# Kernel optimization log

Hardware: AMD Instinct MI355X
Metric: run time of the kernel (lower is better)

## Reference

```python
import jax, jax.numpy as jnp
import numpy as np

B, D, E, H, A = 4096, 1024, 8, 1024, 512  # batch, state_dim, num_options, num_neurons, num_actions


def setup_inputs() -> dict:
    key = jax.random.key(0)
    ks = jax.random.split(key, 16)
    s = 0.02
    return {
        "state": jax.random.normal(ks[0], (B, D), jnp.float32),
        "selected_options": jax.random.randint(ks[1], (B,), 0, E, jnp.int32),
        # option network: Linear(D,H) -> ReLU -> Linear(H,E)
        "Wo1": jax.random.normal(ks[2], (D, H), jnp.float32) * s,
        "bo1": jnp.zeros((H,), jnp.float32),
        "Wo2": jax.random.normal(ks[3], (H, E), jnp.float32) * s,
        "bo2": jnp.zeros((E,), jnp.float32),
        # E expert nets, each: Linear(D,H)+ReLU -> Linear(H,H)+ReLU -> Linear(H,A)
        "We1": jax.random.normal(ks[4], (E, D, H), jnp.float32) * s,
        "be1": jnp.zeros((E, H), jnp.float32),
        "We2": jax.random.normal(ks[5], (E, H, H), jnp.float32) * s,
        "be2": jnp.zeros((E, H), jnp.float32),
        "We3": jax.random.normal(ks[6], (E, H, A), jnp.float32) * s,
        "be3": jnp.zeros((E, A), jnp.float32),
        # termination network: Linear(D,H) -> ReLU -> Linear(H,1) -> Sigmoid
        "Wt1": jax.random.normal(ks[7], (D, H), jnp.float32) * s,
        "bt1": jnp.zeros((H,), jnp.float32),
        "Wt2": jax.random.normal(ks[8], (H, 1), jnp.float32) * s,
        "bt2": jnp.zeros((1,), jnp.float32),
    }


def reference(state, selected_options, Wo1, bo1, Wo2, bo2,
              We1, be1, We2, be2, We3, be3, Wt1, bt1, Wt2, bt2):
    # option head
    option_probs = jax.nn.softmax(jnp.maximum(state @ Wo1 + bo1, 0.0) @ Wo2 + bo2, axis=-1)

    # expert MLPs: compute all experts vectorized, then gather per-sample selected expert.
    # (the torch code loops per sample; equal action sizes so no padding is needed)
    h = jnp.maximum(jnp.einsum("bd,edh->beh", state, We1) + be1, 0.0)   # [B,E,H]
    h = jnp.maximum(jnp.einsum("beh,ehk->bek", h, We2) + be2, 0.0)      # [B,E,H]
    logits = jnp.einsum("beh,eha->bea", h, We3) + be3                   # [B,E,A]
    probs_all = jax.nn.softmax(logits, axis=-1)
    sel = selected_options[:, None, None]
    action_probs = jnp.take_along_axis(probs_all, sel, axis=1)[:, 0, :]  # [B,A]
    selected_actions = jnp.argmax(action_probs, axis=-1)

    # termination head
    termination_prob = jax.nn.sigmoid(jnp.maximum(state @ Wt1 + bt1, 0.0) @ Wt2 + bt2)

    return option_probs, action_probs, termination_prob, selected_options, selected_actions
```

## Files before the change

### kernel.cpp

```cpp
#include <hip/hip_runtime.h>
#include <hip/hip_bf16.h>

#define B_ 4096
#define D_ 1024
#define E_ 8
#define H_ 1024
#define A_ 512
#define PB 6144
#define NTT 24
#define FB_CAP 128
#define FROWS (E_ * FB_CAP)
#define KSPLIT 4
#define MARGIN 3.0e-3f

typedef __attribute__((ext_vector_type(8))) short s16x8;
typedef __attribute__((ext_vector_type(4))) float f32x4;

__device__ __forceinline__ unsigned short f2bf(float f) {
    __hip_bfloat16 h = __float2bfloat16(f);
    return *reinterpret_cast<unsigned short*>(&h);
}
__device__ __forceinline__ float bf2f(unsigned short u) {
    return __uint_as_float(((unsigned int)u) << 16);
}
__device__ __forceinline__ void gload16(const void* g, void* l) {
    __builtin_amdgcn_global_load_lds(
        (const __attribute__((address_space(1))) unsigned int*)g,
        (__attribute__((address_space(3))) unsigned int*)l, 16, 0, 0);
}

__global__ void k_prep(const float* __restrict__ x, unsigned short* __restrict__ y,
                       const float* __restrict__ Wo1, const float* __restrict__ Wt1,
                       unsigned short* __restrict__ Wbf,
                       const int* __restrict__ sel, int* __restrict__ tile_expert,
                       int* __restrict__ rowlist, int* __restrict__ pos_of_row,
                       int* __restrict__ rowlist2, int* __restrict__ cur2) {
    const int t = threadIdx.x;
    if (blockIdx.x > 4096) {
        int j = (blockIdx.x - 4097) * 256 + t;
        float4 v;
        if (j < 262144) v = ((const float4*)Wo1)[j];
        else            v = ((const float4*)Wt1)[j - 262144];
        ushort4 o;
        o.x = f2bf(v.x); o.y = f2bf(v.y); o.z = f2bf(v.z); o.w = f2bf(v.w);
        ((ushort4*)Wbf)[j] = o;
        return;
    }
    if (blockIdx.x > 0) {
        int i = (blockIdx.x - 1) * 256 + t;
        float4 v = ((const float4*)x)[i];
        ushort4 o;
        o.x = f2bf(v.x); o.y = f2bf(v.y); o.z = f2bf(v.z); o.w = f2bf(v.w);
        ((ushort4*)y)[i] = o;
        return;
    }
    __shared__ int scnt[E_], soff[E_], scur[E_];
    if (t < E_) { scnt[t] = 0; scur[t] = 0; cur2[t] = 0; }
    for (int i = t; i < PB; i += 256) rowlist[i] = -1;
    for (int i = t; i < FROWS; i += 256) rowlist2[i] = -1;
    __syncthreads();
    for (int b = t; b < B_; b += 256) {
        int e = sel[b]; e = e < 0 ? 0 : (e >= E_ ? E_ - 1 : e);
        atomicAdd(&scnt[e], 1);
    }
    __syncthreads();
    if (t == 0) {
        int off = 0;
        for (int e = 0; e < E_; ++e) {
            soff[e] = off;
            int tiles = (scnt[e] + 255) >> 8;
            for (int k = 0; k < tiles; ++k) tile_expert[(off >> 8) + k] = e;
            off += tiles << 8;
        }
        for (int k = off >> 8; k < NTT; ++k) tile_expert[k] = -1;
    }
    __syncthreads();
    for (int b = t; b < B_; b += 256) {
        int e = sel[b]; e = e < 0 ? 0 : (e >= E_ ? E_ - 1 : e);
        int pos = atomicAdd(&scur[e], 1);
        int p = soff[e] + pos; if (p >= PB) p = PB - 1;
        rowlist[p] = b;
        pos_of_row[b] = p;
    }
}

template<int TN, int WBF>
__device__ __forceinline__ void gemm2(
    const unsigned short* __restrict__ g0, const unsigned short* __restrict__ g1,
    const unsigned short* __restrict__ g2, const unsigned short* __restrict__ g3,
    const void* __restrict__ Wp, int Nw, const float* __restrict__ bp,
    unsigned short* __restrict__ Cbf, float* __restrict__ Cf, int Ncols, int relu,
    unsigned short* As, unsigned short* Bs)
{
    constexpr int NI = TN / 32;
    constexpr int BL = TN / 8;
    constexpr int BT = TN * 64;
    const int t = threadIdx.x, lane = t & 63, w = t >> 6;
    const int wr = w >> 1, wc = w & 1;
    const int n_loc = t & (TN - 1);
    const int kg = (t / TN) * BL;
    const float* wcolf = (const float*)Wp + n_loc;
    const unsigned short* wcolu = (const unsigned short*)Wp + n_loc;
    const int aseg = w * 2048 + lane * 8;

    f32x4 acc[4][NI];
#pragma unroll
    for (int i = 0; i < 4; ++i)
#pragma unroll
        for (int j = 0; j < NI; ++j)
#pragma unroll
            for (int r = 0; r < 4; ++r) acc[i][j][r] = 0.f;

    float bregf[BL];
    unsigned short bregu[BL];

#define G_STAGE_A(IT, BUF) {                                                 \
        const int o_ = (BUF) * 16384 + aseg;                                 \
        const int ko_ = (IT) * 64;                                           \
        gload16(g0 + ko_, As + o_);                                          \
        gload16(g1 + ko_, As + o_ + 512);                                    \
        gload16(g2 + ko_, As + o_ + 1024);                                   \
        gload16(g3 + ko_, As + o_ + 1536);                                   \
    }

#define G_LOAD_B(IT) {                                                       \
        if constexpr (WBF) {                                                 \
            _Pragma("unroll")                                                \
            for (int i_ = 0; i_ < BL; ++i_)                                  \
                bregu[i_] = wcolu[(size_t)((IT) * 64 + kg + i_) * Nw];       \
        } else {                                                             \
            _Pragma("unroll")                                                \
            for (int i_ = 0; i_ < BL; ++i_)                                  \
                bregf[i_] = wcolf[(size_t)((IT) * 64 + kg + i_) * Nw];       \
        }                                                                    \
    }

#define G_PACK_B(BUF) {                                                      \
        unsigned int u_[BL / 2];                                             \
        if constexpr (WBF) {                                                 \
            _Pragma("unroll")                                                \
            for (int j_ = 0; j_ < BL / 2; ++j_)                              \
                u_[j_] = (unsigned)bregu[2 * j_] | ((unsigned)bregu[2 * j_ + 1] << 16); \
        } else {                                                             \
            _Pragma("unroll")                                                \
            for (int j_ = 0; j_ < BL / 2; ++j_)                              \
                u_[j_] = ((unsigned)f2bf(bregf[2 * j_ + 1]) << 16) | (unsigned)f2bf(bregf[2 * j_]); \
        }                                                                    \
        _Pragma("unroll")                                                    \
        for (int j_ = 0; j_ < BL / 8; ++j_) {                                \
            const int cj_ = (kg >> 3) + j_;                                  \
            uint4 v_;                                                        \
            v_.x = u_[4 * j_]; v_.y = u_[4 * j_ + 1];                        \
            v_.z = u_[4 * j_ + 2]; v_.w = u_[4 * j_ + 3];                    \
            *(uint4*)&Bs[(BUF) * BT + n_loc * 64 + ((cj_ ^ (n_loc & 7)) << 3)] = v_; \
        }                                                                    \
    }

    G_STAGE_A(0, 0);
    G_LOAD_B(0);
    G_PACK_B(0);
    __syncthreads();

    for (int it = 0; it < 16; ++it) {
        const int cb = it & 1;
        if (it + 1 < 16) { G_STAGE_A(it + 1, cb ^ 1); G_LOAD_B(it + 1); }
        __builtin_amdgcn_s_setprio(1);
#pragma unroll
        for (int kq = 0; kq < 2; ++kq) {
            const int sc = kq * 4 + (lane >> 4);
            s16x8 af[4], bfr[NI];
#pragma unroll
            for (int mi = 0; mi < 4; ++mi) {
                const int ar = wr * 64 + mi * 16 + (lane & 15);
                af[mi] = *reinterpret_cast<const s16x8*>(
                    &As[cb * 16384 + ar * 64 + ((sc ^ (ar & 7)) << 3)]);
            }
#pragma unroll
            for (int ni = 0; ni < NI; ++ni) {
                const int br = wc * (TN / 2) + ni * 16 + (lane & 15);
                bfr[ni] = *reinterpret_cast<const s16x8*>(
                    &Bs[cb * BT + br * 64 + ((sc ^ (br & 7)) << 3)]);
            }
#pragma unroll
            for (int mi = 0; mi < 4; ++mi)
#pragma unroll
                for (int ni = 0; ni < NI; ++ni)
                    acc[mi][ni] = __builtin_amdgcn_mfma_f32_16x16x32_bf16(
                        af[mi], bfr[ni], acc[mi][ni], 0, 0, 0);
        }
        __builtin_amdgcn_s_setprio(0);
        if (it + 1 < 16) {
            G_PACK_B(cb ^ 1);
            __syncthreads();
        }
    }
#undef G_PACK_B
#undef G_LOAD_B
#undef G_STAGE_A

    const int cq = lane >> 4, cr = lane & 15;
#pragma unroll
    for (int ni = 0; ni < NI; ++ni) {
        const int col_l = wc * (TN / 2) + ni * 16 + cr;
        const float bv = bp[col_l];
#pragma unroll
        for (int mi = 0; mi < 4; ++mi) {
#pragma unroll
            for (int r = 0; r < 4; ++r) {
                const int row_l = wr * 64 + mi * 16 + cq * 4 + r;
                float v = acc[mi][ni][r] + bv;
                if (relu) v = fmaxf(v, 0.f);
                const size_t idx = (size_t)row_l * Ncols + col_l;
                if (Cbf) Cbf[idx] = f2bf(v);
                if (Cf)  Cf[idx] = v;
            }
        }
    }
}

__device__ __forceinline__ int a_src_chunk(int lane) { return (((lane & 7) ^ (lane >> 3)) * 8); }

__global__ __launch_bounds__(512, 2)
void k_d2(const unsigned short* __restrict__ Sbf,
          const int* __restrict__ rowlist, const int* __restrict__ tile_expert,
          const unsigned short* __restrict__ Wbf,
          const float* __restrict__ bo1, const float* __restrict__ bt1,
          const float* __restrict__ We1, const float* __restrict__ be1,
          unsigned short* __restrict__ hopt, unsigned short* __restrict__ hterm,
          unsigned short* __restrict__ h1) {
    __shared__ __align__(16) unsigned short As[2 * 16384];
    __shared__ __align__(16) unsigned short Bs[2 * 16384];
    const int t = threadIdx.x, lane = t & 63, w = t >> 6;
    const int coff = a_src_chunk(lane);
    const int r0l = w * 32 + (lane >> 3);
    const int bid = blockIdx.x;
    if (bid < 128) {
        const int nt = bid & 7, mt = bid >> 3;
        const unsigned short* g0 = Sbf + (size_t)(mt * 256 + r0l) * D_ + coff;
        const unsigned short* g1 = g0 + (size_t)8 * D_;
        const unsigned short* g2 = g0 + (size_t)16 * D_;
        const unsigned short* g3 = g0 + (size_t)24 * D_;
        const unsigned short* Wp;
        const float* bp;
        unsigned short* C;
        if (nt < 4) { Wp = Wbf + nt * 256; bp = bo1 + nt * 256;
                      C = hopt + (size_t)(mt * 256) * H_ + nt * 256; }
        else { const int n2 = (nt - 4) * 256;
               Wp = Wbf + 1048576 + n2; bp = bt1 + n2;
               C = hterm + (size_t)(mt * 256) * H_ + n2; }
        gemm2<256, 1>(g0, g1, g2, g3, Wp, H_, bp, C, nullptr, H_, 1, As, Bs);
    } else {
        const int q = bid - 128, nt = q & 3, mt = q >> 2;
        const int e = tile_expert[mt]; if (e < 0) return;
        const int base = mt * 256;
        const int sub = rowlist[base]; if (sub < 0) return;
        int r0 = rowlist[base + r0l];      if (r0 < 0) r0 = sub;
        int r1 = rowlist[base + r0l + 8];  if (r1 < 0) r1 = sub;
        int r2 = rowlist[base + r0l + 16]; if (r2 < 0) r2 = sub;
        int r3 = rowlist[base + r0l + 24]; if (r3 < 0) r3 = sub;
        const unsigned short* g0 = Sbf + (size_t)r0 * D_ + coff;
        const unsigned short* g1 = Sbf + (size_t)r1 * D_ + coff;
        const unsigned short* g2 = Sbf + (size_t)r2 * D_ + coff;
        const unsigned short* g3 = Sbf + (size_t)r3 * D_ + coff;
        gemm2<256, 0>(g0, g1, g2, g3,
                      We1 + (size_t)e * D_ * H_ + nt * 256, H_,
                      be1 + (size_t)e * H_ + nt * 256,
                      h1 + (size_t)(mt * 256) * H_ + nt * 256, nullptr, H_, 1, As, Bs);
    }
}

__global__ __launch_bounds__(512, 2)
void k_d3(const unsigned short* __restrict__ h1, const int* __restrict__ tile_expert,
          const float* __restrict__ We2, const float* __restrict__ be2,
          unsigned short* __restrict__ h2) {
    __shared__ __align__(16) unsigned short As[2 * 16384];
    __shared__ __align__(16) unsigned short Bs[2 * 8192];
    const int t = threadIdx.x, lane = t & 63, w = t >> 6;
    const int coff = a_src_chunk(lane);
    const int r0l = w * 32 + (lane >> 3);
    const int nt = blockIdx.x & 7, mt = blockIdx.x >> 3;
    const int e = tile_expert[mt]; if (e < 0) return;
    const unsigned short* g0 = h1 + (size_t)(mt * 256 + r0l) * H_ + coff;
    gemm2<128, 0>(g0, g0 + (size_t)8 * H_, g0 + (size_t)16 * H_, g0 + (size_t)24 * H_,
                  We2 + (size_t)e * H_ * H_ + nt * 128, H_,
                  be2 + (size_t)e * H_ + nt * 128,
                  h2 + (size_t)(mt * 256) * H_ + nt * 128, nullptr, H_, 1, As, Bs);
}

__global__ __launch_bounds__(512, 2)
void k_d5(const unsigned short* __restrict__ h2, const int* __restrict__ tile_expert,
          const float* __restrict__ We3, const float* __restrict__ be3,
          float* __restrict__ lgt) {
    __shared__ __align__(16) unsigned short As[2 * 16384];
    __shared__ __align__(16) unsigned short Bs[2 * 4096];
    const int t = threadIdx.x, lane = t & 63, w = t >> 6;
    const int coff = a_src_chunk(lane);
    const int r0l = w * 32 + (lane >> 3);
    const int nt = blockIdx.x & 7, mt = blockIdx.x >> 3;
    const int e = tile_expert[mt]; if (e < 0) return;
    const unsigned short* g0 = h2 + (size_t)(mt * 256 + r0l) * H_ + coff;
    gemm2<64, 0>(g0, g0 + (size_t)8 * H_, g0 + (size_t)16 * H_, g0 + (size_t)24 * H_,
                 We3 + (size_t)e * H_ * A_ + nt * 64, A_,
                 be3 + (size_t)e * A_ + nt * 64,
                 nullptr, lgt + (size_t)(mt * 256) * A_ + nt * 64, A_, 0, As, Bs);
}

__device__ __forceinline__ void opt_body(int b, const unsigned short* __restrict__ h,
                                         const float* __restrict__ Wo2, const float* __restrict__ bo2,
                                         float* __restrict__ out, float* sm) {
    const int t = threadIdx.x;
    float acc[E_];
#pragma unroll
    for (int j = 0; j < E_; ++j) acc[j] = 0.f;
    for (int k = t; k < H_; k += 256) {
        float hv = bf2f(h[(size_t)b * H_ + k]);
#pragma unroll
        for (int j = 0; j < E_; ++j) acc[j] = fmaf(hv, Wo2[k * E_ + j], acc[j]);
    }
#pragma unroll
    for (int j = 0; j < E_; ++j)
        for (int off = 32; off; off >>= 1) acc[j] += __shfl_down(acc[j], off, 64);
    float* red = sm;
    float* probs = sm + 4 * E_;
    int wave = t >> 6, lane = t & 63;
    if (lane == 0)
        for (int j = 0; j < E_; ++j) red[wave * E_ + j] = acc[j];
    __syncthreads();
    if (t == 0) {
        float z[E_]; float m = -1e30f;
        for (int j = 0; j < E_; ++j) {
            z[j] = red[j] + red[E_ + j] + red[2 * E_ + j] + red[3 * E_ + j] + bo2[j];
            m = fmaxf(m, z[j]);
        }
        float s = 0.f;
        for (int j = 0; j < E_; ++j) { z[j] = expf(z[j] - m); s += z[j]; }
        float inv = 1.f / s;
        for (int j = 0; j < E_; ++j) probs[j] = z[j] * inv;
    }
    __syncthreads();
    if (t < E_) out[(size_t)b * E_ + t] = probs[t];
}

__device__ __forceinline__ void term_body(int b, const unsigned short* __restrict__ h,
                                          const float* __restrict__ Wt2, const float* __restrict__ bt2,
                                          float* __restrict__ out, float* sm) {
    const int t = threadIdx.x;
    float acc = 0.f;
    for (int k = t; k < H_; k += 256) acc = fmaf(bf2f(h[(size_t)b * H_ + k]), Wt2[k], acc);
    for (int off = 32; off; off >>= 1) acc += __shfl_down(acc, off, 64);
    if ((t & 63) == 0) sm[t >> 6] = acc;
    __syncthreads();
    if (t == 0) {
        float z = sm[0] + sm[1] + sm[2] + sm[3] + bt2[0];
        out[b] = 1.f / (1.f + expf(-z));
    }
}

__global__ __launch_bounds__(256)
void k_gather(const float* __restrict__ logits, const int* __restrict__ pos_of_row,
              const int* __restrict__ sel,
              float* __restrict__ out_probs, float* __restrict__ out_selopt,
              float* __restrict__ out_selact,
              int* __restrict__ rowlist2, int* __restrict__ cur2,
              const unsigned short* __restrict__ hopt, const float* __restrict__ Wo2,
              const float* __restrict__ bo2, float* __restrict__ out_opt,
              const unsigned short* __restrict__ hterm, const float* __restrict__ Wt2,
              const float* __restrict__ bt2, float* __restrict__ out_term) {
    __shared__ float smbuf[5 * E_ + 8];
    const int bid = blockIdx.x;
    if (bid >= 2 * B_) { term_body(bid - 2 * B_, hterm, Wt2, bt2, out_term, smbuf); return; }
    if (bid >= B_)     { opt_body(bid - B_, hopt, Wo2, bo2, out_opt, smbuf); return; }

    const int b = bid;
    int p = pos_of_row[b];
    if (p < 0) p = 0; if (p >= PB) p = PB - 1;
    const int t = threadIdx.x;
    const float* L = logits + (size_t)p * A_;
    float v0 = L[t], v1 = L[t + 256];

    float bv; int bi;
    if (v0 >= v1) { bv = v0; bi = t; } else { bv = v1; bi = t + 256; }
    for (int off = 32; off; off >>= 1) {
        float ov = __shfl_down(bv, off, 64);
        int   oi = __shfl_down(bi, off, 64);
        if (ov > bv || (ov == bv && oi < bi)) { bv = ov; bi = oi; }
    }
    __shared__ float rv[4]; __shared__ int ri[4];
    int wave = t >> 6, lane = t & 63;
    if (lane == 0) { rv[wave] = bv; ri[wave] = bi; }
    __syncthreads();
    __shared__ float sM; __shared__ int sBi;
    if (t == 0) {
        float mv = rv[0]; int mi = ri[0];
        for (int w = 1; w < 4; ++w)
            if (rv[w] > mv || (rv[w] == mv && ri[w] < mi)) { mv = rv[w]; mi = ri[w]; }
        sM = mv; sBi = mi;
    }
    __syncthreads();
    const float M = sM; const int BI = sBi;

    float e0 = expf(v0 - M), e1 = expf(v1 - M);
    float s = e0 + e1;
    for (int off = 32; off; off >>= 1) s += __shfl_down(s, off, 64);
    __shared__ float reds[4];
    if (lane == 0) reds[wave] = s;
    __syncthreads();
    float inv = 1.f / (reds[0] + reds[1] + reds[2] + reds[3]);

    out_probs[(size_t)b * A_ + t]       = e0 * inv;
    out_probs[(size_t)b * A_ + t + 256] = e1 * inv;

    float s0 = (t == BI) ? -1e30f : v0;
    float s1 = (t + 256 == BI) ? -1e30f : v1;
    float sm = fmaxf(s0, s1);
    for (int off = 32; off; off >>= 1) sm = fmaxf(sm, __shfl_down(sm, off, 64));
    __shared__ float red2[4];
    if (lane == 0) red2[wave] = sm;
    __syncthreads();

    if (t == 0) {
        float second = fmaxf(fmaxf(red2[0], red2[1]), fmaxf(red2[2], red2[3]));
        out_selact[b] = (float)BI;
        int e = sel[b]; e = e < 0 ? 0 : (e >= E_ ? E_ - 1 : e);
        out_selopt[b] = (float)sel[b];
        if (M - second < MARGIN) {
            int pos = atomicAdd(&cur2[e], 1);
            if (pos < FB_CAP) rowlist2[e * FB_CAP + pos] = b;
        }
    }
}

#define BM 64
#define BN 64
#define BK 32

__global__ __launch_bounds__(256)
void k_pgemm(const float* __restrict__ A, int lda, const int* __restrict__ flags,
             int gather, const float* __restrict__ W,
             float* __restrict__ P, int K, int N) {
    __shared__ float As_[BK][BM + 4];
    __shared__ float Bs_[BK][BN];

    const int mt = blockIdx.y, nt = blockIdx.x, kz = blockIdx.z;
    if (flags[mt * BM] < 0) return;
    const int e = mt >> 1;
    const float* Wb = W + (size_t)e * K * N + (size_t)nt * BN;

    const int t  = threadIdx.x;
    const int tx = t & 15;
    const int ty = t >> 4;

    const int arow = t >> 3;
    const int ak   = (t & 7) * 4;
    int r0 = mt * BM + arow, r1 = r0 + 32;
    if (gather) { r0 = flags[r0]; r1 = flags[r1]; }
    const int bkr = t >> 4;
    const int bn  = (t & 15) * 4;

    float acc[4][4];
#pragma unroll
    for (int i = 0; i < 4; ++i)
#pragma unroll
        for (int j = 0; j < 4; ++j) acc[i][j] = 0.0f;

    const int kbeg = kz * (K / KSPLIT);
    const int kend = kbeg + (K / KSPLIT);
    for (int k0 = kbeg; k0 < kend; k0 += BK) {
        float4 a0 = make_float4(0.f, 0.f, 0.f, 0.f), a1 = a0;
        if (r0 >= 0) a0 = *(const float4*)&A[(size_t)r0 * lda + k0 + ak];
        if (r1 >= 0) a1 = *(const float4*)&A[(size_t)r1 * lda + k0 + ak];
        float4 b0 = *(const float4*)&Wb[(size_t)(k0 + bkr) * N + bn];
        float4 b1 = *(const float4*)&Wb[(size_t)(k0 + bkr + 16) * N + bn];

        __syncthreads();
        As_[ak + 0][arow] = a0.x; As_[ak + 1][arow] = a0.y;
        As_[ak + 2][arow] = a0.z; As_[ak + 3][arow] = a0.w;
        As_[ak + 0][arow + 32] = a1.x; As_[ak + 1][arow + 32] = a1.y;
        As_[ak + 2][arow + 32] = a1.z; As_[ak + 3][arow + 32] = a1.w;
        *(float4*)&Bs_[bkr][bn]      = b0;
        *(float4*)&Bs_[bkr + 16][bn] = b1;
        __syncthreads();

#pragma unroll
        for (int kk = 0; kk < BK; ++kk) {
            const float4 av = *(const float4*)&As_[kk][ty * 4];
            const float4 bv = *(const float4*)&Bs_[kk][tx * 4];
            const float a_[4] = {av.x, av.y, av.z, av.w};
            const float b_[4] = {bv.x, bv.y, bv.z, bv.w};
#pragma unroll
            for (int i = 0; i < 4; ++i)
#pragma unroll
                for (int j = 0; j < 4; ++j)
                    acc[i][j] = fmaf(a_[i], b_[j], acc[i][j]);
        }
    }

    float* Pz = P + (size_t)kz * FROWS * N;
    const int n0 = nt * BN + tx * 4;
#pragma unroll
    for (int i = 0; i < 4; ++i) {
        int m = mt * BM + ty * 4 + i;
        *(float4*)&Pz[(size_t)m * N + n0] = make_float4(acc[i][0], acc[i][1], acc[i][2], acc[i][3]);
    }
}

__global__ __launch_bounds__(256)
void k_fred(const float* __restrict__ P, const int* __restrict__ flags,
            const float* __restrict__ bias, float* __restrict__ C, int N, int relu) {
    const int m = blockIdx.x;
    if (flags[m] < 0) return;
    const int e = m >> 7;
    const int t = threadIdx.x;
    if (t * 4 >= N) return;
    const size_t MN = (size_t)FROWS * N;
    const size_t base = (size_t)m * N + t * 4;
    float4 s = *(const float4*)&P[base];
#pragma unroll
    for (int z = 1; z < KSPLIT; ++z) {
        float4 p = *(const float4*)&P[(size_t)z * MN + base];
        s.x += p.x; s.y += p.y; s.z += p.z; s.w += p.w;
    }
    const float* bp = bias + (size_t)e * N + t * 4;
    s.x += bp[0]; s.y += bp[1]; s.z += bp[2]; s.w += bp[3];
    if (relu) {
        s.x = fmaxf(s.x, 0.f); s.y = fmaxf(s.y, 0.f);
        s.z = fmaxf(s.z, 0.f); s.w = fmaxf(s.w, 0.f);
    }
    *(float4*)&C[base] = s;
}

__global__ __launch_bounds__(256)
void k_fixup(const float* __restrict__ logitsf, const int* __restrict__ rowlist2,
             float* __restrict__ out_probs, float* __restrict__ out_selact) {
    const int i = blockIdx.x;
    const int row = rowlist2[i];
    if (row < 0) return;
    const int t = threadIdx.x;
    const float* L = logitsf + (size_t)i * A_;
    float v0 = L[t], v1 = L[t + 256];

    float bv; int bi;
    if (v0 >= v1) { bv = v0; bi = t; } else { bv = v1; bi = t + 256; }
    for (int off = 32; off; off >>= 1) {
        float ov = __shfl_down(bv, off, 64);
        int   oi = __shfl_down(bi, off, 64);
        if (ov > bv || (ov == bv && oi < bi)) { bv = ov; bi = oi; }
    }
    __shared__ float rv[4]; __shared__ int ri[4];
    int wave = t >> 6, lane = t & 63;
    if (lane == 0) { rv[wave] = bv; ri[wave] = bi; }
    __syncthreads();
    __shared__ float sM; __shared__ int sBi;
    if (t == 0) {
        float mv = rv[0]; int mi = ri[0];
        for (int w = 1; w < 4; ++w)
            if (rv[w] > mv || (rv[w] == mv && ri[w] < mi)) { mv = rv[w]; mi = ri[w]; }
        sM = mv; sBi = mi;
    }
    __syncthreads();

    float e0 = expf(v0 - sM), e1 = expf(v1 - sM);
    float s = e0 + e1;
    for (int off = 32; off; off >>= 1) s += __shfl_down(s, off, 64);
    __shared__ float reds[4];
    if (lane == 0) reds[wave] = s;
    __syncthreads();
    float inv = 1.f / (reds[0] + reds[1] + reds[2] + reds[3]);

    out_probs[(size_t)row * A_ + t]       = e0 * inv;
    out_probs[(size_t)row * A_ + t + 256] = e1 * inv;
    if (t == 0) out_selact[row] = (float)sBi;
}

extern "C" void kernel_launch(void* const* d_in, const int* in_sizes, int n_in,
                              void* d_out, int out_size, void* d_ws, size_t ws_size,
                              hipStream_t stream) {
    const float* state = (const float*)d_in[0];
    const int*   sel   = (const int*)d_in[1];
    const float* Wo1 = (const float*)d_in[2];
    const float* bo1 = (const float*)d_in[3];
    const float* Wo2 = (const float*)d_in[4];
    const float* bo2 = (const float*)d_in[5];
    const float* We1 = (const float*)d_in[6];
    const float* be1 = (const float*)d_in[7];
    const float* We2 = (const float*)d_in[8];
    const float* be2 = (const float*)d_in[9];
    const float* We3 = (const float*)d_in[10];
    const float* be3 = (const float*)d_in[11];
    const float* Wt1 = (const float*)d_in[12];
    const float* bt1 = (const float*)d_in[13];
    const float* Wt2 = (const float*)d_in[14];
    const float* bt2 = (const float*)d_in[15];
    float* out = (float*)d_out;

    char* w = (char*)d_ws;
    int* meta        = (int*)w;
    int* rowlist     = meta;
    int* pos_of_row  = meta + 6144;
    int* rowlist2    = meta + 10240;
    int* tile_expert = meta + 11264;
    int* cur2        = meta + 11296;
    char* P0 = w + 65536;
    char* P1 = P0 + 12582912;
    char* P2 = P1 + 16777216;
    unsigned short* Sbf   = (unsigned short*)P0;
    unsigned short* Wbf   = (unsigned short*)(P0 + (8u << 20));
    unsigned short* h2b   = (unsigned short*)P0;
    unsigned short* hopt  = (unsigned short*)P1;
    unsigned short* hterm = hopt + (size_t)B_ * H_;
    unsigned short* h1b   = (unsigned short*)P2;
    float* lgt  = (float*)P2;
    float* Pbuf = (float*)P1;
    float* h1f  = (float*)P0;
    float* h2f  = h1f + (size_t)FROWS * H_;
    float* lgf  = h2f + (size_t)FROWS * H_;

    size_t act_off    = (size_t)B_ * E_;
    size_t term_off   = act_off + (size_t)B_ * A_;
    size_t selopt_off = term_off + B_;
    size_t selact_off = selopt_off + B_;

    k_prep<<<6145, 256, 0, stream>>>(state, Sbf, Wo1, Wt1, Wbf, sel, tile_expert,
                                     rowlist, pos_of_row, rowlist2, cur2);

    k_d2<<<224, 512, 0, stream>>>(Sbf, rowlist, tile_expert, Wbf,
                                  bo1, bt1, We1, be1, hopt, hterm, h1b);
    k_d3<<<192, 512, 0, stream>>>(h1b, tile_expert, We2, be2, h2b);
    k_d5<<<192, 512, 0, stream>>>(h2b, tile_expert, We3, be3, lgt);

    k_gather<<<3 * B_, 256, 0, stream>>>(lgt, pos_of_row, sel,
                                         out + act_off, out + selopt_off, out + selact_off,
                                         rowlist2, cur2,
                                         hopt, Wo2, bo2, out,
                                         hterm, Wt2, bt2, out + term_off);

    k_pgemm<<<dim3(H_ / BN, FROWS / BM, KSPLIT), 256, 0, stream>>>(state, D_, rowlist2, 1, We1, Pbuf, D_, H_);
    k_fred<<<FROWS, 256, 0, stream>>>(Pbuf, rowlist2, be1, h1f, H_, 1);
    k_pgemm<<<dim3(H_ / BN, FROWS / BM, KSPLIT), 256, 0, stream>>>(h1f, H_, rowlist2, 0, We2, Pbuf, H_, H_);
    k_fred<<<FROWS, 256, 0, stream>>>(Pbuf, rowlist2, be2, h2f, H_, 1);
    k_pgemm<<<dim3(A_ / BN, FROWS / BM, KSPLIT), 256, 0, stream>>>(h2f, H_, rowlist2, 0, We3, Pbuf, H_, A_);
    k_fred<<<FROWS, 256, 0, stream>>>(Pbuf, rowlist2, be3, lgf, A_, 0);
    k_fixup<<<FROWS, 256, 0, stream>>>(lgf, rowlist2, out + act_off, out + selact_off);
}
```

Baseline: 229.6 us.

## Pre-transpose expert weights to bf16 K-major and stage B via direct LDS loads

```diff
diff --git a/kernel.cpp b/kernel.cpp
--- a/kernel.cpp
+++ b/kernel.cpp
@@ -29,25 +29,88 @@
         (__attribute__((address_space(3))) unsigned int*)l, 16, 0, 0);
 }
 
+__device__ __forceinline__ int a_src_chunk(int lane) { return (((lane & 7) ^ (lane >> 3)) * 8); }
+
+__device__ __forceinline__ int trc(int r, int c) { return (c + r + (r >> 2)) & 63; }
+
+__device__ __forceinline__ void tr_tile_256(const float* __restrict__ src, int Nsrc,
+                                            unsigned short* __restrict__ dst, float* T) {
+    const int t = threadIdx.x;
+    const int c4 = (t & 15) * 4, r0 = t >> 4;
+#pragma unroll
+    for (int i = 0; i < 8; ++i) {
+        const int r = r0 + i * 16;
+        const float4 v = *(const float4*)&src[(size_t)r * Nsrc + c4];
+        float* Tr = T + r * 64;
+        Tr[trc(r, c4 + 0)] = v.x; Tr[trc(r, c4 + 1)] = v.y;
+        Tr[trc(r, c4 + 2)] = v.z; Tr[trc(r, c4 + 3)] = v.w;
+    }
+    __syncthreads();
+    const int k4 = (t & 31) * 4, n0 = t >> 5;
+#pragma unroll
+    for (int i = 0; i < 8; ++i) {
+        const int n = n0 + i * 8;
+        ushort4 o;
+        o.x = f2bf(T[(k4 + 0) * 64 + trc(k4 + 0, n)]);
+        o.y = f2bf(T[(k4 + 1) * 64 + trc(k4 + 1, n)]);
+        o.z = f2bf(T[(k4 + 2) * 64 + trc(k4 + 2, n)]);
+        o.w = f2bf(T[(k4 + 3) * 64 + trc(k4 + 3, n)]);
+        *(ushort4*)&dst[(size_t)n * 1024 + k4] = o;
+    }
+}
+
+__device__ __forceinline__ void tr_tile_512(const float* __restrict__ src, int Nsrc,
+                                            unsigned short* __restrict__ dst, float* T) {
+    const int t = threadIdx.x;
+    const int c4 = (t & 15) * 4, r0 = t >> 4;
+#pragma unroll
+    for (int i = 0; i < 8; ++i) {
+        const int r = r0 + i * 32;
+        const float4 v = *(const float4*)&src[(size_t)r * Nsrc + c4];
+        float* Tr = T + r * 64;
+        Tr[trc(r, c4 + 0)] = v.x; Tr[trc(r, c4 + 1)] = v.y;
+        Tr[trc(r, c4 + 2)] = v.z; Tr[trc(r, c4 + 3)] = v.w;
+    }
+    __syncthreads();
+    const int k4 = (t & 63) * 4, n0 = t >> 6;
+#pragma unroll
+    for (int i = 0; i < 8; ++i) {
+        const int n = n0 + i * 8;
+        ushort4 o;
+        o.x = f2bf(T[(k4 + 0) * 64 + trc(k4 + 0, n)]);
+        o.y = f2bf(T[(k4 + 1) * 64 + trc(k4 + 1, n)]);
+        o.z = f2bf(T[(k4 + 2) * 64 + trc(k4 + 2, n)]);
+        o.w = f2bf(T[(k4 + 3) * 64 + trc(k4 + 3, n)]);
+        *(ushort4*)&dst[(size_t)n * 1024 + k4] = o;
+    }
+}
+
 __global__ void k_prep(const float* __restrict__ x, unsigned short* __restrict__ y,
                        const float* __restrict__ Wo1, const float* __restrict__ Wt1,
                        unsigned short* __restrict__ Wbf,
+                       const float* __restrict__ We1, unsigned short* __restrict__ We1t,
                        const int* __restrict__ sel, int* __restrict__ tile_expert,
                        int* __restrict__ rowlist, int* __restrict__ pos_of_row,
                        int* __restrict__ rowlist2, int* __restrict__ cur2) {
-    const int t = threadIdx.x;
-    if (blockIdx.x > 4096) {
-        int j = (blockIdx.x - 4097) * 256 + t;
-        float4 v;
-        if (j < 262144) v = ((const float4*)Wo1)[j];
-        else            v = ((const float4*)Wt1)[j - 262144];
-        ushort4 o;
-        o.x = f2bf(v.x); o.y = f2bf(v.y); o.z = f2bf(v.z); o.w = f2bf(v.w);
-        ((ushort4*)Wbf)[j] = o;
+    __shared__ float T[128 * 64];
+    const int t = threadIdx.x;
+    const int bid = blockIdx.x;
+    if (bid >= 4353) {
+        const int q = bid - 4353;
+        const int e = q >> 7, r = q & 127, kt = r >> 4, ntb = r & 15;
+        tr_tile_256(We1 + (size_t)e * 1048576 + (size_t)(kt * 128) * 1024 + ntb * 64, 1024,
+                    We1t + (size_t)e * 1048576 + (size_t)(ntb * 64) * 1024 + kt * 128, T);
         return;
     }
-    if (blockIdx.x > 0) {
-        int i = (blockIdx.x - 1) * 256 + t;
+    if (bid >= 4097) {
+        const int q = bid - 4097;
+        const int m = q >> 7, r = q & 127, kt = r >> 4, ntb = r & 15;
+        const float* src = (m ? Wt1 : Wo1) + (size_t)(kt * 128) * 1024 + ntb * 64;
+        tr_tile_256(src, 1024, Wbf + (size_t)(m * 1024 + ntb * 64) * 1024 + kt * 128, T);
+        return;
+    }
+    if (bid > 0) {
+        int i = (bid - 1) * 256 + t;
         float4 v = ((const float4*)x)[i];
         ushort4 o;
         o.x = f2bf(v.x); o.y = f2bf(v.y); o.z = f2bf(v.z); o.w = f2bf(v.w);
@@ -84,24 +147,23 @@
     }
 }
 
-template<int TN, int WBF>
-__device__ __forceinline__ void gemm2(
+template<int TN>
+__device__ __forceinline__ void gemm3(
     const unsigned short* __restrict__ g0, const unsigned short* __restrict__ g1,
     const unsigned short* __restrict__ g2, const unsigned short* __restrict__ g3,
-    const void* __restrict__ Wp, int Nw, const float* __restrict__ bp,
+    const unsigned short* __restrict__ Bt, int Kg, const float* __restrict__ bp,
     unsigned short* __restrict__ Cbf, float* __restrict__ Cf, int Ncols, int relu,
     unsigned short* As, unsigned short* Bs)
 {
     constexpr int NI = TN / 32;
-    constexpr int BL = TN / 8;
-    constexpr int BT = TN * 64;
+    constexpr int BTH = TN * 64;
+    constexpr int BR = TN / 64;
     const int t = threadIdx.x, lane = t & 63, w = t >> 6;
     const int wr = w >> 1, wc = w & 1;
-    const int n_loc = t & (TN - 1);
-    const int kg = (t / TN) * BL;
-    const float* wcolf = (const float*)Wp + n_loc;
-    const unsigned short* wcolu = (const unsigned short*)Wp + n_loc;
     const int aseg = w * 2048 + lane * 8;
+    const int bseg = w * (BR * 512) + lane * 8;
+    const int coffb = a_src_chunk(lane);
+    const unsigned short* bsrc = Bt + (size_t)(w * BR * 8 + (lane >> 3)) * Kg + coffb;
 
     f32x4 acc[4][NI];
 #pragma unroll
@@ -111,59 +173,25 @@
 #pragma unroll
             for (int r = 0; r < 4; ++r) acc[i][j][r] = 0.f;
 
-    float bregf[BL];
-    unsigned short bregu[BL];
-
-#define G_STAGE_A(IT, BUF) {                                                 \
-        const int o_ = (BUF) * 16384 + aseg;                                 \
+#define G_STAGE(IT, BUF) {                                                   \
         const int ko_ = (IT) * 64;                                           \
-        gload16(g0 + ko_, As + o_);                                          \
-        gload16(g1 + ko_, As + o_ + 512);                                    \
-        gload16(g2 + ko_, As + o_ + 1024);                                   \
-        gload16(g3 + ko_, As + o_ + 1536);                                   \
-    }
-
-#define G_LOAD_B(IT) {                                                       \
-        if constexpr (WBF) {                                                 \
-            _Pragma("unroll")                                                \
-            for (int i_ = 0; i_ < BL; ++i_)                                  \
-                bregu[i_] = wcolu[(size_t)((IT) * 64 + kg + i_) * Nw];       \
-        } else {                                                             \
-            _Pragma("unroll")                                                \
-            for (int i_ = 0; i_ < BL; ++i_)                                  \
-                bregf[i_] = wcolf[(size_t)((IT) * 64 + kg + i_) * Nw];       \
-        }                                                                    \
-    }
-
-#define G_PACK_B(BUF) {                                                      \
-        unsigned int u_[BL / 2];                                             \
-        if constexpr (WBF) {                                                 \
-            _Pragma("unroll")                                                \
-            for (int j_ = 0; j_ < BL / 2; ++j_)                              \
-                u_[j_] = (unsigned)bregu[2 * j_] | ((unsigned)bregu[2 * j_ + 1] << 16); \
-        } else {                                                             \
-            _Pragma("unroll")                                                \
-            for (int j_ = 0; j_ < BL / 2; ++j_)                              \
-                u_[j_] = ((unsigned)f2bf(bregf[2 * j_ + 1]) << 16) | (unsigned)f2bf(bregf[2 * j_]); \
-        }                                                                    \
+        const int oa_ = (BUF) * 16384 + aseg;                                \
+        gload16(g0 + ko_, As + oa_);                                         \
+        gload16(g1 + ko_, As + oa_ + 512);                                   \
+        gload16(g2 + ko_, As + oa_ + 1024);                                  \
+        gload16(g3 + ko_, As + oa_ + 1536);                                  \
+        const int ob_ = (BUF) * BTH + bseg;                                  \
         _Pragma("unroll")                                                    \
-        for (int j_ = 0; j_ < BL / 8; ++j_) {                                \
-            const int cj_ = (kg >> 3) + j_;                                  \
-            uint4 v_;                                                        \
-            v_.x = u_[4 * j_]; v_.y = u_[4 * j_ + 1];                        \
-            v_.z = u_[4 * j_ + 2]; v_.w = u_[4 * j_ + 3];                    \
-            *(uint4*)&Bs[(BUF) * BT + n_loc * 64 + ((cj_ ^ (n_loc & 7)) << 3)] = v_; \
-        }                                                                    \
-    }
-
-    G_STAGE_A(0, 0);
-    G_LOAD_B(0);
-    G_PACK_B(0);
+        for (int j_ = 0; j_ < BR; ++j_)                                      \
+            gload16(bsrc + ko_ + (size_t)(j_ * 8) * Kg, Bs + ob_ + j_ * 512); \
+    }
+
+    G_STAGE(0, 0);
     __syncthreads();
 
     for (int it = 0; it < 16; ++it) {
         const int cb = it & 1;
-        if (it + 1 < 16) { G_STAGE_A(it + 1, cb ^ 1); G_LOAD_B(it + 1); }
+        if (it + 1 < 16) G_STAGE(it + 1, cb ^ 1);
         __builtin_amdgcn_s_setprio(1);
 #pragma unroll
         for (int kq = 0; kq < 2; ++kq) {
@@ -179,7 +207,7 @@
             for (int ni = 0; ni < NI; ++ni) {
                 const int br = wc * (TN / 2) + ni * 16 + (lane & 15);
                 bfr[ni] = *reinterpret_cast<const s16x8*>(
-                    &Bs[cb * BT + br * 64 + ((sc ^ (br & 7)) << 3)]);
+                    &Bs[cb * BTH + br * 64 + ((sc ^ (br & 7)) << 3)]);
             }
 #pragma unroll
             for (int mi = 0; mi < 4; ++mi)
@@ -189,14 +217,9 @@
                         af[mi], bfr[ni], acc[mi][ni], 0, 0, 0);
         }
         __builtin_amdgcn_s_setprio(0);
-        if (it + 1 < 16) {
-            G_PACK_B(cb ^ 1);
-            __syncthreads();
-        }
-    }
-#undef G_PACK_B
-#undef G_LOAD_B
-#undef G_STAGE_A
+        if (it + 1 < 16) __syncthreads();
+    }
+#undef G_STAGE
 
     const int cq = lane >> 4, cr = lane & 15;
 #pragma unroll
@@ -218,37 +241,43 @@
     }
 }
 
-__device__ __forceinline__ int a_src_chunk(int lane) { return (((lane & 7) ^ (lane >> 3)) * 8); }
-
 __global__ __launch_bounds__(512, 2)
 void k_d2(const unsigned short* __restrict__ Sbf,
           const int* __restrict__ rowlist, const int* __restrict__ tile_expert,
           const unsigned short* __restrict__ Wbf,
           const float* __restrict__ bo1, const float* __restrict__ bt1,
-          const float* __restrict__ We1, const float* __restrict__ be1,
+          const unsigned short* __restrict__ We1t, const float* __restrict__ be1,
+          const float* __restrict__ We2, unsigned short* __restrict__ We2t,
           unsigned short* __restrict__ hopt, unsigned short* __restrict__ hterm,
           unsigned short* __restrict__ h1) {
-    __shared__ __align__(16) unsigned short As[2 * 16384];
-    __shared__ __align__(16) unsigned short Bs[2 * 16384];
+    __shared__ __align__(16) unsigned short SMEM[4 * 16384];
+    unsigned short* As = SMEM;
+    unsigned short* Bs = SMEM + 2 * 16384;
+    const int bid = blockIdx.x;
+    if (bid >= 224) {
+        const int q = bid - 224;
+        const int e = q >> 6, r = q & 63, kt = r >> 4, ntb = r & 15;
+        tr_tile_512(We2 + (size_t)e * 1048576 + (size_t)(kt * 256) * 1024 + ntb * 64, 1024,
+                    We2t + (size_t)e * 1048576 + (size_t)(ntb * 64) * 1024 + kt * 256,
+                    (float*)SMEM);
+        return;
+    }
     const int t = threadIdx.x, lane = t & 63, w = t >> 6;
     const int coff = a_src_chunk(lane);
     const int r0l = w * 32 + (lane >> 3);
-    const int bid = blockIdx.x;
     if (bid < 128) {
         const int nt = bid & 7, mt = bid >> 3;
         const unsigned short* g0 = Sbf + (size_t)(mt * 256 + r0l) * D_ + coff;
         const unsigned short* g1 = g0 + (size_t)8 * D_;
         const unsigned short* g2 = g0 + (size_t)16 * D_;
         const unsigned short* g3 = g0 + (size_t)24 * D_;
-        const unsigned short* Wp;
-        const float* bp;
-        unsigned short* C;
-        if (nt < 4) { Wp = Wbf + nt * 256; bp = bo1 + nt * 256;
+        int ntRow; const float* bp; unsigned short* C;
+        if (nt < 4) { ntRow = nt * 256; bp = bo1 + nt * 256;
                       C = hopt + (size_t)(mt * 256) * H_ + nt * 256; }
-        else { const int n2 = (nt - 4) * 256;
-               Wp = Wbf + 1048576 + n2; bp = bt1 + n2;
-               C = hterm + (size_t)(mt * 256) * H_ + n2; }
-        gemm2<256, 1>(g0, g1, g2, g3, Wp, H_, bp, C, nullptr, H_, 1, As, Bs);
+        else { ntRow = 1024 + (nt - 4) * 256; bp = bt1 + (nt - 4) * 256;
+               C = hterm + (size_t)(mt * 256) * H_ + (nt - 4) * 256; }
+        gemm3<256>(g0, g1, g2, g3, Wbf + (size_t)ntRow * 1024, 1024, bp,
+                   C, nullptr, H_, 1, As, Bs);
     } else {
         const int q = bid - 128, nt = q & 3, mt = q >> 2;
         const int e = tile_expert[mt]; if (e < 0) return;
@@ -262,47 +291,59 @@
         const unsigned short* g1 = Sbf + (size_t)r1 * D_ + coff;
         const unsigned short* g2 = Sbf + (size_t)r2 * D_ + coff;
         const unsigned short* g3 = Sbf + (size_t)r3 * D_ + coff;
-        gemm2<256, 0>(g0, g1, g2, g3,
-                      We1 + (size_t)e * D_ * H_ + nt * 256, H_,
-                      be1 + (size_t)e * H_ + nt * 256,
-                      h1 + (size_t)(mt * 256) * H_ + nt * 256, nullptr, H_, 1, As, Bs);
+        gemm3<256>(g0, g1, g2, g3,
+                   We1t + (size_t)e * 1048576 + (size_t)(nt * 256) * 1024, 1024,
+                   be1 + (size_t)e * H_ + nt * 256,
+                   h1 + (size_t)(mt * 256) * H_ + nt * 256, nullptr, H_, 1, As, Bs);
     }
 }
 
 __global__ __launch_bounds__(512, 2)
 void k_d3(const unsigned short* __restrict__ h1, const int* __restrict__ tile_expert,
-          const float* __restrict__ We2, const float* __restrict__ be2,
+          const unsigned short* __restrict__ We2t, const float* __restrict__ be2,
+          const float* __restrict__ We3, unsigned short* __restrict__ We3t,
           unsigned short* __restrict__ h2) {
-    __shared__ __align__(16) unsigned short As[2 * 16384];
-    __shared__ __align__(16) unsigned short Bs[2 * 8192];
+    __shared__ __align__(16) unsigned short SMEM[2 * 16384 + 2 * 8192];
+    unsigned short* As = SMEM;
+    unsigned short* Bs = SMEM + 2 * 16384;
+    const int bid = blockIdx.x;
+    if (bid >= 192) {
+        const int q = bid - 192;
+        const int e = q >> 5, r = q & 31, kt = r >> 3, ntb = r & 7;
+        tr_tile_512(We3 + (size_t)e * 524288 + (size_t)(kt * 256) * 512 + ntb * 64, 512,
+                    We3t + (size_t)e * 524288 + (size_t)(ntb * 64) * 1024 + kt * 256,
+                    (float*)SMEM);
+        return;
+    }
     const int t = threadIdx.x, lane = t & 63, w = t >> 6;
     const int coff = a_src_chunk(lane);
     const int r0l = w * 32 + (lane >> 3);
-    const int nt = blockIdx.x & 7, mt = blockIdx.x >> 3;
+    const int nt = bid & 7, mt = bid >> 3;
     const int e = tile_expert[mt]; if (e < 0) return;
     const unsigned short* g0 = h1 + (size_t)(mt * 256 + r0l) * H_ + coff;
-    gemm2<128, 0>(g0, g0 + (size_t)8 * H_, g0 + (size_t)16 * H_, g0 + (size_t)24 * H_,
-                  We2 + (size_t)e * H_ * H_ + nt * 128, H_,
-                  be2 + (size_t)e * H_ + nt * 128,
-                  h2 + (size_t)(mt * 256) * H_ + nt * 128, nullptr, H_, 1, As, Bs);
+    gemm3<128>(g0, g0 + (size_t)8 * H_, g0 + (size_t)16 * H_, g0 + (size_t)24 * H_,
+               We2t + (size_t)e * 1048576 + (size_t)(nt * 128) * 1024, 1024,
+               be2 + (size_t)e * H_ + nt * 128,
+               h2 + (size_t)(mt * 256) * H_ + nt * 128, nullptr, H_, 1, As, Bs);
 }
 
 __global__ __launch_bounds__(512, 2)
 void k_d5(const unsigned short* __restrict__ h2, const int* __restrict__ tile_expert,
-          const float* __restrict__ We3, const float* __restrict__ be3,
+          const unsigned short* __restrict__ We3t, const float* __restrict__ be3,
           float* __restrict__ lgt) {
-    __shared__ __align__(16) unsigned short As[2 * 16384];
-    __shared__ __align__(16) unsigned short Bs[2 * 4096];
+    __shared__ __align__(16) unsigned short SMEM[2 * 16384 + 2 * 4096];
+    unsigned short* As = SMEM;
+    unsigned short* Bs = SMEM + 2 * 16384;
     const int t = threadIdx.x, lane = t & 63, w = t >> 6;
     const int coff = a_src_chunk(lane);
     const int r0l = w * 32 + (lane >> 3);
     const int nt = blockIdx.x & 7, mt = blockIdx.x >> 3;
     const int e = tile_expert[mt]; if (e < 0) return;
     const unsigned short* g0 = h2 + (size_t)(mt * 256 + r0l) * H_ + coff;
-    gemm2<64, 0>(g0, g0 + (size_t)8 * H_, g0 + (size_t)16 * H_, g0 + (size_t)24 * H_,
-                 We3 + (size_t)e * H_ * A_ + nt * 64, A_,
-                 be3 + (size_t)e * A_ + nt * 64,
-                 nullptr, lgt + (size_t)(mt * 256) * A_ + nt * 64, A_, 0, As, Bs);
+    gemm3<64>(g0, g0 + (size_t)8 * H_, g0 + (size_t)16 * H_, g0 + (size_t)24 * H_,
+              We3t + (size_t)e * 524288 + (size_t)(nt * 64) * 1024, 1024,
+              be3 + (size_t)e * A_ + nt * 64,
+              nullptr, lgt + (size_t)(mt * 256) * A_ + nt * 64, A_, 0, As, Bs);
 }
 
 __device__ __forceinline__ void opt_body(int b, const unsigned short* __restrict__ h,
@@ -603,12 +644,17 @@
     char* P0 = w + 65536;
     char* P1 = P0 + 12582912;
     char* P2 = P1 + 16777216;
+    char* W1 = P2 + 12582912;
+    char* W2 = W1 + 16777216;
     unsigned short* Sbf   = (unsigned short*)P0;
     unsigned short* Wbf   = (unsigned short*)(P0 + (8u << 20));
     unsigned short* h2b   = (unsigned short*)P0;
     unsigned short* hopt  = (unsigned short*)P1;
     unsigned short* hterm = hopt + (size_t)B_ * H_;
     unsigned short* h1b   = (unsigned short*)P2;
+    unsigned short* We1t  = (unsigned short*)W1;
+    unsigned short* We3t  = (unsigned short*)W1;
+    unsigned short* We2t  = (unsigned short*)W2;
     float* lgt  = (float*)P2;
     float* Pbuf = (float*)P1;
     float* h1f  = (float*)P0;
@@ -620,13 +666,13 @@
     size_t selopt_off = term_off + B_;
     size_t selact_off = selopt_off + B_;
 
-    k_prep<<<6145, 256, 0, stream>>>(state, Sbf, Wo1, Wt1, Wbf, sel, tile_expert,
-                                     rowlist, pos_of_row, rowlist2, cur2);
-
-    k_d2<<<224, 512, 0, stream>>>(Sbf, rowlist, tile_expert, Wbf,
-                                  bo1, bt1, We1, be1, hopt, hterm, h1b);
-    k_d3<<<192, 512, 0, stream>>>(h1b, tile_expert, We2, be2, h2b);
-    k_d5<<<192, 512, 0, stream>>>(h2b, tile_expert, We3, be3, lgt);
+    k_prep<<<5377, 256, 0, stream>>>(state, Sbf, Wo1, Wt1, Wbf, We1, We1t,
+                                     sel, tile_expert, rowlist, pos_of_row, rowlist2, cur2);
+
+    k_d2<<<736, 512, 0, stream>>>(Sbf, rowlist, tile_expert, Wbf,
+                                  bo1, bt1, We1t, be1, We2, We2t, hopt, hterm, h1b);
+    k_d3<<<448, 512, 0, stream>>>(h1b, tile_expert, We2t, be2, We3, We3t, h2b);
+    k_d5<<<192, 512, 0, stream>>>(h2b, tile_expert, We3t, be3, lgt);
 
     k_gather<<<3 * B_, 256, 0, stream>>>(lgt, pos_of_row, sel,
                                          out + act_off, out + selopt_off, out + selact_off,
```

Measured after the change: 208.2 us. -9.3%, faster.
